# Optimization experiments

Hardware: AMD Instinct MI355X
Metric: run time of the kernel (lower is better)

## Reference

```python
import jax, jax.numpy as jnp
import numpy as np

B, N, F, S, OUT = 8, 12000, 128, 16, 128

def setup_inputs() -> dict:
    key = jax.random.key(0)
    k1, k2, k3, k4 = jax.random.split(key, 4)
    x = jax.random.normal(k1, (B, N, F), dtype=jnp.float32)
    # Linear(in_c*spiral_size, out_c): weight [out, in], bias [out]
    bound = 1.0 / np.sqrt(F * S)
    W = jax.random.uniform(k2, (OUT, F * S), dtype=jnp.float32, minval=-bound, maxval=bound)
    b = jax.random.uniform(k3, (OUT,), dtype=jnp.float32, minval=-bound, maxval=bound)
    spiral_adj = jax.random.randint(k4, (1, N, S), 0, N, dtype=jnp.int32)
    zero_padding = jnp.ones((1, N, 1), dtype=jnp.float32)
    return {"x": x, "W": W, "b": b, "spiral_adj": spiral_adj, "zero_padding": zero_padding}

def reference(x, W, b, spiral_adj, zero_padding):
    # x: [B, N, F]; spiral_adj: [1, N, S] vertex indices shared across batch
    idx = spiral_adj[0]                         # [N, S]
    spirals = x[:, idx, :]                      # [B, N, S, F] gather along vertex dim
    bsz, npts, s, f = spirals.shape
    spirals = spirals.reshape(bsz, npts, s * f)  # [B, N, S*F]
    out = jnp.einsum('bnk,ok->bno', spirals, W) + b  # [B, N, OUT]
    out = jax.nn.relu(out)
    return out * zero_padding
```

## Files before the change

### kernel.cpp

```cpp
#include <hip/hip_runtime.h>

#define BATCH 8
#define NPTS  12000
#define FDIM  128
#define SDIM  16
#define ODIM  128
#define KDIM  (SDIM * FDIM)
#define MTOT  (BATCH * NPTS)

#define BM 128
#define BK 64

#define NTILES 94
#define XELEMS (BATCH * NPTS * FDIM)
#define WELEMS (ODIM * KDIM)
#define XBYTES ((size_t)XELEMS * 2)
#define WBYTES ((size_t)WELEMS * 2)

#define SCW 68

typedef __bf16 bf16x4 __attribute__((ext_vector_type(4)));
typedef __bf16 bf16x8 __attribute__((ext_vector_type(8)));
typedef float  f32x4  __attribute__((ext_vector_type(4)));
typedef float  f32x8  __attribute__((ext_vector_type(8)));

#define AS1(p) ((const __attribute__((address_space(1))) void*)(p))
#define AS3(p) ((__attribute__((address_space(3))) void*)(p))

#define CVT_XBLK 6000
#define CVT_WBLK 128
#define CVT_BPB  750

__global__ __launch_bounds__(256)
void cvt_f32_bf16(const float* __restrict__ x, const float* __restrict__ W,
                  __bf16* __restrict__ xb, __bf16* __restrict__ Wb) {
    const int blk = blockIdx.x;
    const float* __restrict__ src;
    __bf16* __restrict__ dst;
    size_t base;
    if (blk < CVT_XBLK) {
        const int b = blk & 7;
        const int c = blk >> 3;
        base = ((size_t)b * CVT_BPB + c) * (256 * 8) + (size_t)threadIdx.x * 8;
        src = x;  dst = xb;
    } else {
        base = (size_t)(blk - CVT_XBLK) * (256 * 8) + (size_t)threadIdx.x * 8;
        src = W;  dst = Wb;
    }
    const f32x8 v = *reinterpret_cast<const f32x8*>(src + base);
    bf16x8 h;
#pragma unroll
    for (int e = 0; e < 8; ++e) h[e] = (__bf16)v[e];
    *reinterpret_cast<bf16x8*>(dst + base) = h;
}

__global__ __launch_bounds__(512, 4)
void spiral_gemm_bf16(const __bf16* __restrict__ xb,
                      const __bf16* __restrict__ Wb,
                      const float*  __restrict__ bias,
                      const int*    __restrict__ idx,
                      const float*  __restrict__ zp,
                      float*        __restrict__ out)
{
    __shared__ char smem[73728];
    auto As = reinterpret_cast<__bf16(*)[BM * BK]>(smem);
    auto Ws = reinterpret_cast<__bf16(*)[ODIM * BK]>(smem + 32768);
    int*   idxS    = reinterpret_cast<int*>(smem + 65536);
    float* scratch = reinterpret_cast<float*>(smem);

    const int tid   = threadIdx.x;
    const int wave  = tid >> 6;
    const int lane  = tid & 63;
    const int batch = blockIdx.x & 7;
    const int n0    = (blockIdx.x >> 3) * BM;

    const int lrow8 = lane >> 3;
    const int clog  = (lane & 7) ^ lrow8;

    const __bf16* xbase = xb + (size_t)batch * (NPTS * FDIM);

    {
        const int row  = tid >> 2, q4 = tid & 3;
        const int n    = n0 + row;
        const int nrow = n < NPTS ? n : NPTS - 1;
        const int4* s4 = reinterpret_cast<const int4*>(idx + nrow * SDIM + q4 * 4);
        int4* d4       = reinterpret_cast<int4*>(&idxS[row * SDIM + q4 * 4]);
        d4[0] = s4[0];
    }
    __syncthreads();

    int rrow[2];
#pragma unroll
    for (int p = 0; p < 2; ++p) rrow[p] = (p * 8 + wave) * 8 + lrow8;

    int gCur[2], gNext[2];
#pragma unroll
    for (int p = 0; p < 2; ++p) gCur[p] = idxS[rrow[p] * SDIM + 0];

    auto issue = [&](int buf, int kt, const int* g) {
        const int f0 = (kt & 1) * BK;
#pragma unroll
        for (int p = 0; p < 2; ++p) {
            const int r0 = (p * 8 + wave) * 8;
            const __bf16* ga = xbase + (size_t)g[p] * FDIM + f0 + clog * 8;
            __builtin_amdgcn_global_load_lds(AS1(ga), AS3(&As[buf][r0 * BK]), 16, 0, 0);
            const __bf16* gw = Wb + (size_t)(r0 + lrow8) * KDIM + kt * BK + clog * 8;
            __builtin_amdgcn_global_load_lds(AS1(gw), AS3(&Ws[buf][r0 * BK]), 16, 0, 0);
        }
    };

    f32x4 acc[4][4];
#pragma unroll
    for (int i = 0; i < 4; ++i)
#pragma unroll
        for (int j = 0; j < 4; ++j)
            acc[i][j] = f32x4{0.f, 0.f, 0.f, 0.f};

    const int q    = wave >> 1;
    const int kkw  = wave & 1;
    const int wm   = (q >> 1) * 64;
    const int wn   = (q & 1) * 64;
    const int lrow = lane & 15;
    const int quad = lane >> 4;
    const int ph   = (kkw * 4 + quad) ^ (lrow & 7);

    auto compute = [&](int buf) {
        bf16x8 a[4], b[4];
#pragma unroll
        for (int i = 0; i < 4; ++i)
            a[i] = *reinterpret_cast<const bf16x8*>(
                &As[buf][(wm + i * 16 + lrow) * BK + ph * 8]);
#pragma unroll
        for (int j = 0; j < 4; ++j)
            b[j] = *reinterpret_cast<const bf16x8*>(
                &Ws[buf][(wn + j * 16 + lrow) * BK + ph * 8]);
#pragma unroll
        for (int i = 0; i < 4; ++i)
#pragma unroll
            for (int j = 0; j < 4; ++j)
                acc[i][j] = __builtin_amdgcn_mfma_f32_16x16x32_bf16(
                    a[i], b[j], acc[i][j], 0, 0, 0);
    };

    issue(0, 0, gCur);

    for (int t = 0; t < 16; ++t) {
        issue(1, 2 * t + 1, gCur);
        asm volatile("s_waitcnt vmcnt(4)" ::: "memory");
        asm volatile("s_barrier" ::: "memory");
        if (t < 15) {
#pragma unroll
            for (int p = 0; p < 2; ++p)
                gNext[p] = idxS[rrow[p] * SDIM + t + 1];
        }
        compute(0);
        asm volatile("s_barrier" ::: "memory");

        if (t < 15) {
            issue(0, 2 * t + 2, gNext);
            asm volatile("s_waitcnt vmcnt(4)" ::: "memory");
        } else {
            asm volatile("s_waitcnt vmcnt(0)" ::: "memory");
        }
        asm volatile("s_barrier" ::: "memory");
        compute(1);
        asm volatile("s_barrier" ::: "memory");
#pragma unroll
        for (int p = 0; p < 2; ++p) gCur[p] = gNext[p];
    }

    __syncthreads();
    float* sc = scratch + q * (64 * SCW);
    if (kkw == 1) {
#pragma unroll
        for (int i = 0; i < 4; ++i)
#pragma unroll
            for (int j = 0; j < 4; ++j)
                *reinterpret_cast<f32x4*>(
                    &sc[(j * 16 + lrow) * SCW + i * 16 + quad * 4]) = acc[i][j];
    }
    __syncthreads();
    if (kkw == 0) {
#pragma unroll
        for (int i = 0; i < 4; ++i)
#pragma unroll
            for (int j = 0; j < 4; ++j)
                acc[i][j] += *reinterpret_cast<const f32x4*>(
                    &sc[(j * 16 + lrow) * SCW + i * 16 + quad * 4]);

#pragma unroll
        for (int i = 0; i < 4; ++i) {
#pragma unroll
            for (int r = 0; r < 4; ++r) {
                const int row = wm + i * 16 + quad * 4 + r;
                const int n   = n0 + row;
                if (n < NPTS) {
                    const float z = zp[n];
                    float* orow   = out + ((size_t)batch * NPTS + n) * ODIM;
#pragma unroll
                    for (int j = 0; j < 4; ++j) {
                        const int col = wn + j * 16 + lrow;
                        float v = acc[i][j][r] + bias[col];
                        v = fmaxf(v, 0.f);
                        orow[col] = v * z;
                    }
                }
            }
        }
    }
}

#define LDA 72
#define BMF 128
__global__ __launch_bounds__(256, 2)
void spiral_gemm_fp32(const float* __restrict__ x, const float* __restrict__ W,
                      const float* __restrict__ bias, const int* __restrict__ idx,
                      const float* __restrict__ zp, float* __restrict__ out)
{
    __shared__ __bf16 Asf[BMF * LDA];
    __shared__ __bf16 Wsf[ODIM * LDA];
    const int tid = threadIdx.x, wave = tid >> 6, lane = tid & 63;
    const int m0 = blockIdx.x * BMF;
    const int srow = tid >> 3, schunk = tid & 7;
    int a_n[4]; const float* a_xb[4];
#pragma unroll
    for (int p = 0; p < 4; ++p) {
        int m = m0 + srow + p * 32, bb = m / NPTS;
        a_n[p] = m - bb * NPTS; a_xb[p] = x + (size_t)bb * (NPTS * FDIM);
    }
    f32x4 acc[4][4];
#pragma unroll
    for (int i = 0; i < 4; ++i)
#pragma unroll
        for (int j = 0; j < 4; ++j) acc[i][j] = f32x4{0.f,0.f,0.f,0.f};
    const int wm = (wave >> 1) * 64, wn = (wave & 1) * 64;
    const int lrow = lane & 15, quad = lane >> 4;
    for (int kt = 0; kt < KDIM / 64; ++kt) {
        const int s = kt >> 1, f0 = (kt & 1) * 64;
        __syncthreads();
#pragma unroll
        for (int p = 0; p < 4; ++p) {
            const int r = srow + p * 32;
            const int g = idx[a_n[p] * SDIM + s];
            const f32x8 v = *reinterpret_cast<const f32x8*>(
                a_xb[p] + (size_t)g * FDIM + f0 + schunk * 8);
            bf16x8 h;
#pragma unroll
            for (int e = 0; e < 8; ++e) h[e] = (__bf16)v[e];
            *reinterpret_cast<bf16x8*>(&Asf[r * LDA + schunk * 8]) = h;
            const f32x8 w = *reinterpret_cast<const f32x8*>(
                W + (size_t)r * KDIM + kt * 64 + schunk * 8);
            bf16x8 hw;
#pragma unroll
            for (int e = 0; e < 8; ++e) hw[e] = (__bf16)w[e];
            *reinterpret_cast<bf16x8*>(&Wsf[r * LDA + schunk * 8]) = hw;
        }
        __syncthreads();
#pragma unroll
        for (int kk = 0; kk < 2; ++kk) {
            const int koff = kk * 32 + quad * 8;
            bf16x8 a[4], b[4];
#pragma unroll
            for (int i = 0; i < 4; ++i)
                a[i] = *reinterpret_cast<const bf16x8*>(&Asf[(wm + i*16 + lrow)*LDA + koff]);
#pragma unroll
            for (int j = 0; j < 4; ++j)
                b[j] = *reinterpret_cast<const bf16x8*>(&Wsf[(wn + j*16 + lrow)*LDA + koff]);
#pragma unroll
            for (int i = 0; i < 4; ++i)
#pragma unroll
                for (int j = 0; j < 4; ++j)
                    acc[i][j] = __builtin_amdgcn_mfma_f32_16x16x32_bf16(a[i], b[j], acc[i][j], 0,0,0);
        }
    }
#pragma unroll
    for (int i = 0; i < 4; ++i)
#pragma unroll
        for (int r = 0; r < 4; ++r) {
            const int row = wm + i * 16 + quad * 4 + r;
            const int m = m0 + row, bb = m / NPTS, nnn = m - bb * NPTS;
            const float z = zp[nnn];
            float* orow = out + (size_t)m * ODIM;
#pragma unroll
            for (int j = 0; j < 4; ++j) {
                const int col = wn + j * 16 + lrow;
                float v = acc[i][j][r] + bias[col];
                orow[col] = fmaxf(v, 0.f) * z;
            }
        }
}

extern "C" void kernel_launch(void* const* d_in, const int* in_sizes, int n_in,
                              void* d_out, int out_size, void* d_ws, size_t ws_size,
                              hipStream_t stream) {
    const float* x    = (const float*)d_in[0];
    const float* W    = (const float*)d_in[1];
    const float* bias = (const float*)d_in[2];
    const int*   idx  = (const int*)d_in[3];
    const float* zp   = (const float*)d_in[4];
    float*       out  = (float*)d_out;

    if (ws_size >= XBYTES + WBYTES) {
        __bf16* xb = (__bf16*)d_ws;
        __bf16* Wb = (__bf16*)((char*)d_ws + XBYTES);
        cvt_f32_bf16<<<dim3(CVT_XBLK + CVT_WBLK), dim3(256), 0, stream>>>(x, W, xb, Wb);
        spiral_gemm_bf16<<<dim3(BATCH * NTILES), dim3(512), 0, stream>>>(
            xb, Wb, bias, idx, zp, out);
    } else {
        spiral_gemm_fp32<<<dim3(MTOT / BMF), dim3(256), 0, stream>>>(
            x, W, bias, idx, zp, out);
    }
}
```

Measured before the change: 157.8 us.

## Load gathered A fragments directly from global memory, dropping A LDS staging

Removes the LDS double-buffer for the gathered x tile. Each wave now reads its bf16x8 A fragments straight from global memory, using the per-row spiral indices it holds in registers, while W stays staged through LDS with async loads. This cuts LDS traffic and shared-memory footprint for A. In exchange, global-load latency lands inside the compute loop with no prefetch, and waves sharing the same rows load the same data twice.

```diff
diff --git a/kernel.cpp b/kernel.cpp
--- a/kernel.cpp
+++ b/kernel.cpp
@@ -63,9 +63,8 @@
                       float*        __restrict__ out)
 {
     __shared__ char smem[73728];
-    auto As = reinterpret_cast<__bf16(*)[BM * BK]>(smem);
-    auto Ws = reinterpret_cast<__bf16(*)[ODIM * BK]>(smem + 32768);
-    int*   idxS    = reinterpret_cast<int*>(smem + 65536);
+    auto Ws = reinterpret_cast<__bf16(*)[ODIM * BK]>(smem);
+    int*   idxS    = reinterpret_cast<int*>(smem + 32768);
     float* scratch = reinterpret_cast<float*>(smem);
 
     const int tid   = threadIdx.x;
@@ -89,33 +88,6 @@
     }
     __syncthreads();
 
-    int rrow[2];
-#pragma unroll
-    for (int p = 0; p < 2; ++p) rrow[p] = (p * 8 + wave) * 8 + lrow8;
-
-    int gCur[2], gNext[2];
-#pragma unroll
-    for (int p = 0; p < 2; ++p) gCur[p] = idxS[rrow[p] * SDIM + 0];
-
-    auto issue = [&](int buf, int kt, const int* g) {
-        const int f0 = (kt & 1) * BK;
-#pragma unroll
-        for (int p = 0; p < 2; ++p) {
-            const int r0 = (p * 8 + wave) * 8;
-            const __bf16* ga = xbase + (size_t)g[p] * FDIM + f0 + clog * 8;
-            __builtin_amdgcn_global_load_lds(AS1(ga), AS3(&As[buf][r0 * BK]), 16, 0, 0);
-            const __bf16* gw = Wb + (size_t)(r0 + lrow8) * KDIM + kt * BK + clog * 8;
-            __builtin_amdgcn_global_load_lds(AS1(gw), AS3(&Ws[buf][r0 * BK]), 16, 0, 0);
-        }
-    };
-
-    f32x4 acc[4][4];
-#pragma unroll
-    for (int i = 0; i < 4; ++i)
-#pragma unroll
-        for (int j = 0; j < 4; ++j)
-            acc[i][j] = f32x4{0.f, 0.f, 0.f, 0.f};
-
     const int q    = wave >> 1;
     const int kkw  = wave & 1;
     const int wm   = (q >> 1) * 64;
@@ -124,12 +96,38 @@
     const int quad = lane >> 4;
     const int ph   = (kkw * 4 + quad) ^ (lrow & 7);
 
-    auto compute = [&](int buf) {
+    int arow[4];
+#pragma unroll
+    for (int i = 0; i < 4; ++i) arow[i] = wm + i * 16 + lrow;
+
+    int gCurA[4], gNextA[4];
+#pragma unroll
+    for (int i = 0; i < 4; ++i) gCurA[i] = idxS[arow[i] * SDIM + 0];
+
+    auto issueW = [&](int buf, int kt) {
+#pragma unroll
+        for (int p = 0; p < 2; ++p) {
+            const int r0 = (p * 8 + wave) * 8;
+            const __bf16* gw = Wb + (size_t)(r0 + lrow8) * KDIM + kt * BK + clog * 8;
+            __builtin_amdgcn_global_load_lds(AS1(gw), AS3(&Ws[buf][r0 * BK]), 16, 0, 0);
+        }
+    };
+
+    f32x4 acc[4][4];
+#pragma unroll
+    for (int i = 0; i < 4; ++i)
+#pragma unroll
+        for (int j = 0; j < 4; ++j)
+            acc[i][j] = f32x4{0.f, 0.f, 0.f, 0.f};
+
+    const int acol = kkw * 32 + quad * 8;
+
+    auto compute = [&](int buf, int f0, const int* gA) {
         bf16x8 a[4], b[4];
 #pragma unroll
         for (int i = 0; i < 4; ++i)
             a[i] = *reinterpret_cast<const bf16x8*>(
-                &As[buf][(wm + i * 16 + lrow) * BK + ph * 8]);
+                xbase + (size_t)gA[i] * FDIM + f0 + acol);
 #pragma unroll
         for (int j = 0; j < 4; ++j)
             b[j] = *reinterpret_cast<const bf16x8*>(
@@ -142,31 +140,31 @@
                     a[i], b[j], acc[i][j], 0, 0, 0);
     };
 
-    issue(0, 0, gCur);
+    issueW(0, 0);
 
     for (int t = 0; t < 16; ++t) {
-        issue(1, 2 * t + 1, gCur);
-        asm volatile("s_waitcnt vmcnt(4)" ::: "memory");
+        issueW(1, 2 * t + 1);
+        asm volatile("s_waitcnt vmcnt(2)" ::: "memory");
         asm volatile("s_barrier" ::: "memory");
         if (t < 15) {
 #pragma unroll
-            for (int p = 0; p < 2; ++p)
-                gNext[p] = idxS[rrow[p] * SDIM + t + 1];
-        }
-        compute(0);
+            for (int i = 0; i < 4; ++i)
+                gNextA[i] = idxS[arow[i] * SDIM + t + 1];
+        }
+        compute(0, 0, gCurA);
         asm volatile("s_barrier" ::: "memory");
 
         if (t < 15) {
-            issue(0, 2 * t + 2, gNext);
-            asm volatile("s_waitcnt vmcnt(4)" ::: "memory");
+            issueW(0, 2 * t + 2);
+            asm volatile("s_waitcnt vmcnt(2)" ::: "memory");
         } else {
             asm volatile("s_waitcnt vmcnt(0)" ::: "memory");
         }
         asm volatile("s_barrier" ::: "memory");
-        compute(1);
+        compute(1, 64, gCurA);
         asm volatile("s_barrier" ::: "memory");
 #pragma unroll
-        for (int p = 0; p < 2; ++p) gCur[p] = gNext[p];
+        for (int i = 0; i < 4; ++i) gCurA[i] = gNextA[i];
     }
 
     __syncthreads();
```

After: 241.1 us. 1.53x slower.
